# Performance work log

Hardware: AMD Instinct MI355X
Metric: run time of the kernel (lower is better)

The kernel has to match this reference:

```python
import jax, jax.numpy as jnp
import numpy as np

NUM_NODES = 50000
NUM_EDGES = 600000
IN_DIM = 128
OUT_DIM = 128


def setup_inputs() -> dict:
    key = jax.random.key(0)
    k1, k2, k3, k4, k5 = jax.random.split(key, 5)
    x = jax.random.normal(k1, (NUM_NODES, IN_DIM), dtype=jnp.float32)
    edge_index = jax.random.randint(k2, (2, NUM_EDGES), 0, NUM_NODES, dtype=jnp.int64)
    edge_weight = jax.random.uniform(k3, (NUM_EDGES,), dtype=jnp.float32)
    W = jax.random.normal(k4, (OUT_DIM, IN_DIM), dtype=jnp.float32) * (1.0 / np.sqrt(IN_DIM))
    b = jax.random.normal(k5, (OUT_DIM,), dtype=jnp.float32) * 0.01
    return {"x": x, "edge_index": edge_index, "edge_weight": edge_weight, "W": W, "b": b}


def reference(x, edge_index, edge_weight, W, b):
    num_nodes = x.shape[0]
    # add self loops
    loop = jnp.arange(num_nodes, dtype=edge_index.dtype)
    src = jnp.concatenate([edge_index[0], loop])           # [E + N]
    tgt = jnp.concatenate([edge_index[1], loop])           # [E + N]
    w = jnp.concatenate([edge_weight, jnp.ones((num_nodes,), dtype=edge_weight.dtype)])
    # degree via scatter-add over src, then symmetric normalization
    deg = jax.ops.segment_sum(w, src, num_segments=num_nodes)  # [N]
    dinv = 1.0 / jnp.sqrt(deg)
    w_norm = w * dinv[src] * dinv[tgt]                      # [E + N]
    # gather-scale-scatter aggregation
    msg = x[src] * w_norm[:, None]                          # [E + N, D]
    agg = jax.ops.segment_sum(msg, tgt, num_segments=num_nodes)  # [N, D]
    # dense linear (torch Linear convention)
    return agg @ W.T + b
```

## Files before the change

kernel.cpp:

```cpp
#include <hip/hip_runtime.h>

#define D 128
#define GROWS 32
#define HCHUNKS 64
#define RNG_H 8064
#define RNG_S 16128


__device__ __forceinline__ unsigned bf16rne(float f) {
  unsigned u = __float_as_uint(f);
  return (u + 0x7FFFu + ((u >> 16) & 1u)) >> 16;
}

__device__ __forceinline__ float4 bf16x4(uint2 u) {
  float4 r;
  r.x = __uint_as_float(u.x << 16);
  r.y = __uint_as_float(u.x & 0xFFFF0000u);
  r.z = __uint_as_float(u.y << 16);
  r.w = __uint_as_float(u.y & 0xFFFF0000u);
  return r;
}

__global__ __launch_bounds__(256) void k_setup(const float* __restrict__ W,
                                               const int* __restrict__ ei,
                                               float* __restrict__ Wt,
                                               int* __restrict__ flag) {
  int i = blockIdx.x * 256 + threadIdx.x;
  if (i < D * D) {
    int c = i >> 7, k = i & 127;
    Wt[k * D + c] = W[i];
  }
  if (i == 0) {
    flag[0] = (ei[1] == 0 && ei[3] == 0 && ei[5] == 0 && ei[7] == 0) ? 1 : 0;
  }
}

__global__ __launch_bounds__(256) void k_gemm(const float* __restrict__ x,
                                              const float* __restrict__ Wt,
                                              uint2* __restrict__ yb,
                                              int N) {
  __shared__ float Xs[GROWS * D];
  const int tid = threadIdx.x;
  const int row0 = blockIdx.x * GROWS;

  for (int f = tid; f < GROWS * D / 4; f += 256) {
    int r = row0 + ((f * 4) >> 7);
    float4 v = make_float4(0.f, 0.f, 0.f, 0.f);
    if (r < N)
      v = reinterpret_cast<const float4*>(x)[(size_t)row0 * (D / 4) + f];
    reinterpret_cast<float4*>(Xs)[f] = v;
  }
  __syncthreads();

  const int c0 = (tid & 31) * 4;
  const int r0 = (tid >> 5) * 4;
  float acc[4][4];
#pragma unroll
  for (int i = 0; i < 4; ++i)
#pragma unroll
    for (int j = 0; j < 4; ++j) acc[i][j] = 0.f;

#pragma unroll 4
  for (int k = 0; k < D; ++k) {
    float4 wv = reinterpret_cast<const float4*>(Wt)[(k * D + c0) >> 2];
    float xr[4];
#pragma unroll
    for (int i = 0; i < 4; ++i) xr[i] = Xs[(r0 + i) * D + k];
#pragma unroll
    for (int i = 0; i < 4; ++i) {
      acc[i][0] += xr[i] * wv.x;
      acc[i][1] += xr[i] * wv.y;
      acc[i][2] += xr[i] * wv.z;
      acc[i][3] += xr[i] * wv.w;
    }
  }
#pragma unroll
  for (int i = 0; i < 4; ++i) {
    int row = row0 + r0 + i;
    if (row < N) {
      uint2 u;
      u.x = bf16rne(acc[i][0]) | (bf16rne(acc[i][1]) << 16);
      u.y = bf16rne(acc[i][2]) | (bf16rne(acc[i][3]) << 16);
      yb[(size_t)row * 32 + (tid & 31)] = u;
    }
  }
}

__global__ __launch_bounds__(256) void k_hist(const int* __restrict__ ei,
                                              const float* __restrict__ ew,
                                              float* __restrict__ pdeg,
                                              int* __restrict__ pcnt,
                                              const int* __restrict__ flag,
                                              int E) {
  __shared__ float hd[RNG_H];
  __shared__ int hc[RNG_H];
  const int tid = threadIdx.x;
  const int chunk = blockIdx.x, r = blockIdx.y;
  const int lo = r * RNG_H;
  for (int i = tid; i < RNG_H; i += 256) { hd[i] = 0.f; hc[i] = 0; }
  __syncthreads();

  const int epc = (E + HCHUNKS - 1) / HCHUNKS;
  const int e0 = chunk * epc;
  const int e1 = min(e0 + epc, E);
  const bool f64 = flag[0] != 0;
  const int2* ei2 = reinterpret_cast<const int2*>(ei);
  for (int e = e0 + tid; e < e1; e += 256) {
    int s = f64 ? ei2[e].x : ei[e];
    int t = f64 ? ei2[E + e].x : ei[E + e];
    int ds = s - lo;
    if ((unsigned)ds < (unsigned)RNG_H) atomicAdd(&hd[ds], ew[e]);
    int dt = t - lo;
    if ((unsigned)dt < (unsigned)RNG_H) atomicAdd(&hc[dt], 1);
  }
  __syncthreads();
  size_t base = ((size_t)r * HCHUNKS + chunk) * RNG_H;
  for (int i = tid; i < RNG_H; i += 256) {
    pdeg[base + i] = hd[i];
    pcnt[base + i] = hc[i];
  }
}

__device__ __forceinline__ int wave_incl_scan(int v, int lane) {
#pragma unroll
  for (int o = 1; o < 64; o <<= 1) {
    int t = __shfl_up(v, o);
    if (lane >= o) v += t;
  }
  return v;
}

__global__ __launch_bounds__(256) void k_scan1(const float* __restrict__ pdeg,
                                               const int* __restrict__ pcnt,
                                               float* __restrict__ dinv,
                                               int* __restrict__ rowptr,
                                               int* __restrict__ blocksum,
                                               int N) {
  __shared__ int wtot[4];
  int tid = threadIdx.x;
  int i = blockIdx.x * 256 + tid;
  int v = 0;
  if (i < N) {
    int r = i / RNG_H, off = i - r * RNG_H;
    size_t base = (size_t)r * HCHUNKS * RNG_H + off;
    float s = 0.f;
    int c = 0;
#pragma unroll 8
    for (int k = 0; k < HCHUNKS; ++k) {
      s += pdeg[base + (size_t)k * RNG_H];
      c += pcnt[base + (size_t)k * RNG_H];
    }
    dinv[i] = rsqrtf(s + 1.0f);
    v = c;
  }
  int lane = tid & 63, wv = tid >> 6;
  int inc = wave_incl_scan(v, lane);
  if (lane == 63) wtot[wv] = inc;
  __syncthreads();
  if (tid == 0) {
    int r = 0;
#pragma unroll
    for (int k = 0; k < 4; ++k) { int t = wtot[k]; wtot[k] = r; r += t; }
  }
  __syncthreads();
  int exc = wtot[wv] + inc - v;
  if (i < N) rowptr[i] = exc;
  if (tid == 255) blocksum[blockIdx.x] = wtot[3] + inc;
}

__global__ __launch_bounds__(64) void k_scan2(int* __restrict__ blocksum,
                                              int* __restrict__ blockoff,
                                              int nb) {
  int lane = threadIdx.x;
  int carry = 0;
  for (int base = 0; base < nb; base += 64) {
    int idx = base + lane;
    int v = (idx < nb) ? blocksum[idx] : 0;
    int inc = wave_incl_scan(v, lane);
    if (idx < nb) blockoff[idx] = carry + inc - v;
    carry += __shfl(inc, 63);
  }
}

__global__ __launch_bounds__(256) void k_scan3base(int* __restrict__ rowptr,
                                                   const int* __restrict__ blockoff,
                                                   const int* __restrict__ pcnt,
                                                   int* __restrict__ cbase,
                                                   int N, int E) {
  int i = blockIdx.x * 256 + threadIdx.x;
  if (i >= N) {
    if (i == N) rowptr[N] = E;
    return;
  }
  int rp = rowptr[i] + blockoff[blockIdx.x];
  rowptr[i] = rp;
  if (i == 0) rowptr[N] = E;
  int r = i / RNG_H, off = i - r * RNG_H;
  size_t pb = (size_t)r * HCHUNKS * RNG_H + off;
  int run = rp;
#pragma unroll 8
  for (int c = 0; c < HCHUNKS; ++c) {
    cbase[(size_t)c * N + i] = run;
    run += pcnt[pb + (size_t)c * RNG_H];
  }
}

__global__ __launch_bounds__(256) void k_scatter(const int* __restrict__ ei,
                                                 const float* __restrict__ ew,
                                                 const float* __restrict__ dinv,
                                                 const int* __restrict__ cbase,
                                                 int2* __restrict__ edges,
                                                 const int* __restrict__ flag,
                                                 int N, int E) {
  __shared__ int hb[RNG_S];
  const int tid = threadIdx.x;
  const int chunk = blockIdx.x, r = blockIdx.y;
  const int lo = r * RNG_S;
  for (int j = tid; j < RNG_S; j += 256) {
    int v = lo + j;
    hb[j] = (v < N) ? cbase[(size_t)chunk * N + v] : 0;
  }
  __syncthreads();

  const int epc = (E + HCHUNKS - 1) / HCHUNKS;
  const int e0 = chunk * epc;
  const int e1 = min(e0 + epc, E);
  const bool f64 = flag[0] != 0;
  const int2* ei2 = reinterpret_cast<const int2*>(ei);
  for (int e = e0 + tid; e < e1; e += 256) {
    int t = f64 ? ei2[E + e].x : ei[E + e];
    int dt = t - lo;
    if ((unsigned)dt < (unsigned)RNG_S) {
      int s = f64 ? ei2[e].x : ei[e];
      int pos = atomicAdd(&hb[dt], 1);
      edges[pos] = make_int2(s, __float_as_int(ew[e] * dinv[s]));
    }
  }
}

__global__ __launch_bounds__(256) void k_gather(const int* __restrict__ rowptr,
                                                const int2* __restrict__ edges,
                                                const uint2* __restrict__ yb,
                                                const float* __restrict__ dinv,
                                                const float* __restrict__ b,
                                                float* __restrict__ out,
                                                int N) {
  const int tid = threadIdx.x;
  const int node = blockIdx.x * 4 + (tid >> 6);
  if (node >= N) return;
  const int lane = tid & 63, half = lane >> 5, l32 = lane & 31;

  const float dt = dinv[node];
  const float4 yself = bf16x4(yb[(size_t)node * 32 + l32]);
  const float4 bb = reinterpret_cast<const float4*>(b)[l32];

  float4 acc = make_float4(0.f, 0.f, 0.f, 0.f);
  const int end = rowptr[node + 1];
  int e = rowptr[node] + half;
  for (; e + 6 < end; e += 8) {
    int2 e0 = edges[e], e1 = edges[e + 2], e2 = edges[e + 4], e3 = edges[e + 6];
    float4 v0 = bf16x4(yb[(size_t)e0.x * 32 + l32]);
    float4 v1 = bf16x4(yb[(size_t)e1.x * 32 + l32]);
    float4 v2 = bf16x4(yb[(size_t)e2.x * 32 + l32]);
    float4 v3 = bf16x4(yb[(size_t)e3.x * 32 + l32]);
    float w0 = __int_as_float(e0.y), w1 = __int_as_float(e1.y);
    float w2 = __int_as_float(e2.y), w3 = __int_as_float(e3.y);
    acc.x += w0 * v0.x; acc.y += w0 * v0.y; acc.z += w0 * v0.z; acc.w += w0 * v0.w;
    acc.x += w1 * v1.x; acc.y += w1 * v1.y; acc.z += w1 * v1.z; acc.w += w1 * v1.w;
    acc.x += w2 * v2.x; acc.y += w2 * v2.y; acc.z += w2 * v2.z; acc.w += w2 * v2.w;
    acc.x += w3 * v3.x; acc.y += w3 * v3.y; acc.z += w3 * v3.z; acc.w += w3 * v3.w;
  }
  for (; e < end; e += 2) {
    int2 e0 = edges[e];
    float4 v0 = bf16x4(yb[(size_t)e0.x * 32 + l32]);
    float w0 = __int_as_float(e0.y);
    acc.x += w0 * v0.x; acc.y += w0 * v0.y; acc.z += w0 * v0.z; acc.w += w0 * v0.w;
  }
  acc.x += __shfl(acc.x, l32 + 32);
  acc.y += __shfl(acc.y, l32 + 32);
  acc.z += __shfl(acc.z, l32 + 32);
  acc.w += __shfl(acc.w, l32 + 32);
  if (half == 0) {
    float4 r;
    r.x = bb.x + dt * (acc.x + dt * yself.x);
    r.y = bb.y + dt * (acc.y + dt * yself.y);
    r.z = bb.z + dt * (acc.z + dt * yself.z);
    r.w = bb.w + dt * (acc.w + dt * yself.w);
    reinterpret_cast<float4*>(out)[(size_t)node * 32 + l32] = r;
  }
}

extern "C" void kernel_launch(void* const* d_in, const int* in_sizes, int n_in,
                              void* d_out, int out_size, void* d_ws, size_t ws_size,
                              hipStream_t stream) {
  const float* x = (const float*)d_in[0];
  const int* ei = (const int*)d_in[1];
  const float* ew = (const float*)d_in[2];
  const float* W = (const float*)d_in[3];
  const float* b = (const float*)d_in[4];
  float* out = (float*)d_out;

  const int N = in_sizes[0] / D;
  const int E = in_sizes[2];
  const int NB = (N + 255) / 256;
  const int nrH = (N + RNG_H - 1) / RNG_H;
  const int nrS = (N + RNG_S - 1) / RNG_S;

  char* ws = (char*)d_ws;
  size_t off = 0;
  auto alloc = [&](size_t bytes) {
    char* p = ws + off;
    off = (off + bytes + 255) & ~(size_t)255;
    return p;
  };
  float* Wt = (float*)alloc((size_t)D * D * 4);
  uint2* yb = (uint2*)alloc((size_t)N * D * 2);
  float* dinv = (float*)alloc((size_t)N * 4);
  float* pdeg = (float*)alloc((size_t)nrH * HCHUNKS * RNG_H * 4);
  int* pcnt = (int*)alloc((size_t)nrH * HCHUNKS * RNG_H * 4);
  int* cbase = (int*)alloc((size_t)HCHUNKS * N * 4);
  int* rowptr = (int*)alloc((size_t)(N + 1) * 4);
  int* blocksum = (int*)alloc((size_t)NB * 4);
  int* blockoff = (int*)alloc((size_t)NB * 4);
  int2* edges = (int2*)alloc((size_t)E * 8);
  int* flag = (int*)alloc(4);

  hipLaunchKernelGGL(k_setup, dim3((D * D + 255) / 256), dim3(256), 0, stream,
                     W, ei, Wt, flag);
  hipLaunchKernelGGL(k_gemm, dim3((N + GROWS - 1) / GROWS), dim3(256), 0,
                     stream, x, Wt, yb, N);
  hipLaunchKernelGGL(k_hist, dim3(HCHUNKS, nrH), dim3(256), 0, stream,
                     ei, ew, pdeg, pcnt, flag, E);
  hipLaunchKernelGGL(k_scan1, dim3(NB), dim3(256), 0, stream,
                     pdeg, pcnt, dinv, rowptr, blocksum, N);
  hipLaunchKernelGGL(k_scan2, dim3(1), dim3(64), 0, stream,
                     blocksum, blockoff, NB);
  hipLaunchKernelGGL(k_scan3base, dim3(NB), dim3(256), 0, stream,
                     rowptr, blockoff, pcnt, cbase, N, E);
  hipLaunchKernelGGL(k_scatter, dim3(HCHUNKS, nrS), dim3(256), 0, stream,
                     ei, ew, dinv, cbase, edges, flag, N, E);
  hipLaunchKernelGGL(k_gather, dim3((N + 3) / 4), dim3(256), 0, stream,
                     rowptr, edges, yb, dinv, b, out, N);
}
```

Baseline: 229.8 us.

## Double edge chunks, unify histogram/scatter node ranges, store partial counts as u16

Raises the number of edge chunks from 64 to 128 and gives the scatter kernel the same node range as the histogram kernel, so both launch more blocks. Per-chunk partial counts are now stored as 16-bit values, which halves the traffic for that buffer. The rowptr[N] write is moved to an extra scan block. In exchange, the per-chunk cbase and pdeg buffers double in size, scan1 and scan3base loop over twice as many chunks, and each scatter block re-reads its edge chunk for more node ranges.

```diff
diff --git a/kernel.cpp b/kernel.cpp
--- a/kernel.cpp
+++ b/kernel.cpp
@@ -2,9 +2,8 @@
 
 #define D 128
 #define GROWS 32
-#define HCHUNKS 64
-#define RNG_H 8064
-#define RNG_S 16128
+#define HCHUNKS 128
+#define RNG 8064
 
 
 __device__ __forceinline__ unsigned bf16rne(float f) {
@@ -89,15 +88,15 @@
 __global__ __launch_bounds__(256) void k_hist(const int* __restrict__ ei,
                                               const float* __restrict__ ew,
                                               float* __restrict__ pdeg,
-                                              int* __restrict__ pcnt,
+                                              unsigned short* __restrict__ pcnt,
                                               const int* __restrict__ flag,
                                               int E) {
-  __shared__ float hd[RNG_H];
-  __shared__ int hc[RNG_H];
+  __shared__ float hd[RNG];
+  __shared__ int hc[RNG];
   const int tid = threadIdx.x;
   const int chunk = blockIdx.x, r = blockIdx.y;
-  const int lo = r * RNG_H;
-  for (int i = tid; i < RNG_H; i += 256) { hd[i] = 0.f; hc[i] = 0; }
+  const int lo = r * RNG;
+  for (int i = tid; i < RNG; i += 256) { hd[i] = 0.f; hc[i] = 0; }
   __syncthreads();
 
   const int epc = (E + HCHUNKS - 1) / HCHUNKS;
@@ -109,15 +108,15 @@
     int s = f64 ? ei2[e].x : ei[e];
     int t = f64 ? ei2[E + e].x : ei[E + e];
     int ds = s - lo;
-    if ((unsigned)ds < (unsigned)RNG_H) atomicAdd(&hd[ds], ew[e]);
+    if ((unsigned)ds < (unsigned)RNG) atomicAdd(&hd[ds], ew[e]);
     int dt = t - lo;
-    if ((unsigned)dt < (unsigned)RNG_H) atomicAdd(&hc[dt], 1);
-  }
-  __syncthreads();
-  size_t base = ((size_t)r * HCHUNKS + chunk) * RNG_H;
-  for (int i = tid; i < RNG_H; i += 256) {
+    if ((unsigned)dt < (unsigned)RNG) atomicAdd(&hc[dt], 1);
+  }
+  __syncthreads();
+  size_t base = ((size_t)r * HCHUNKS + chunk) * RNG;
+  for (int i = tid; i < RNG; i += 256) {
     pdeg[base + i] = hd[i];
-    pcnt[base + i] = hc[i];
+    pcnt[base + i] = (unsigned short)hc[i];
   }
 }
 
@@ -131,7 +130,7 @@
 }
 
 __global__ __launch_bounds__(256) void k_scan1(const float* __restrict__ pdeg,
-                                               const int* __restrict__ pcnt,
+                                               const unsigned short* __restrict__ pcnt,
                                                float* __restrict__ dinv,
                                                int* __restrict__ rowptr,
                                                int* __restrict__ blocksum,
@@ -141,14 +140,14 @@
   int i = blockIdx.x * 256 + tid;
   int v = 0;
   if (i < N) {
-    int r = i / RNG_H, off = i - r * RNG_H;
-    size_t base = (size_t)r * HCHUNKS * RNG_H + off;
+    int r = i / RNG, off = i - r * RNG;
+    size_t base = (size_t)r * HCHUNKS * RNG + off;
     float s = 0.f;
     int c = 0;
 #pragma unroll 8
     for (int k = 0; k < HCHUNKS; ++k) {
-      s += pdeg[base + (size_t)k * RNG_H];
-      c += pcnt[base + (size_t)k * RNG_H];
+      s += pdeg[base + (size_t)k * RNG];
+      c += pcnt[base + (size_t)k * RNG];
     }
     dinv[i] = rsqrtf(s + 1.0f);
     v = c;
@@ -184,7 +183,7 @@
 
 __global__ __launch_bounds__(256) void k_scan3base(int* __restrict__ rowptr,
                                                    const int* __restrict__ blockoff,
-                                                   const int* __restrict__ pcnt,
+                                                   const unsigned short* __restrict__ pcnt,
                                                    int* __restrict__ cbase,
                                                    int N, int E) {
   int i = blockIdx.x * 256 + threadIdx.x;
@@ -194,14 +193,13 @@
   }
   int rp = rowptr[i] + blockoff[blockIdx.x];
   rowptr[i] = rp;
-  if (i == 0) rowptr[N] = E;
-  int r = i / RNG_H, off = i - r * RNG_H;
-  size_t pb = (size_t)r * HCHUNKS * RNG_H + off;
+  int r = i / RNG, off = i - r * RNG;
+  size_t pb = (size_t)r * HCHUNKS * RNG + off;
   int run = rp;
 #pragma unroll 8
   for (int c = 0; c < HCHUNKS; ++c) {
     cbase[(size_t)c * N + i] = run;
-    run += pcnt[pb + (size_t)c * RNG_H];
+    run += pcnt[pb + (size_t)c * RNG];
   }
 }
 
@@ -212,11 +210,11 @@
                                                  int2* __restrict__ edges,
                                                  const int* __restrict__ flag,
                                                  int N, int E) {
-  __shared__ int hb[RNG_S];
+  __shared__ int hb[RNG];
   const int tid = threadIdx.x;
   const int chunk = blockIdx.x, r = blockIdx.y;
-  const int lo = r * RNG_S;
-  for (int j = tid; j < RNG_S; j += 256) {
+  const int lo = r * RNG;
+  for (int j = tid; j < RNG; j += 256) {
     int v = lo + j;
     hb[j] = (v < N) ? cbase[(size_t)chunk * N + v] : 0;
   }
@@ -230,7 +228,7 @@
   for (int e = e0 + tid; e < e1; e += 256) {
     int t = f64 ? ei2[E + e].x : ei[E + e];
     int dt = t - lo;
-    if ((unsigned)dt < (unsigned)RNG_S) {
+    if ((unsigned)dt < (unsigned)RNG) {
       int s = f64 ? ei2[e].x : ei[e];
       int pos = atomicAdd(&hb[dt], 1);
       edges[pos] = make_int2(s, __float_as_int(ew[e] * dinv[s]));
@@ -303,8 +301,7 @@
   const int N = in_sizes[0] / D;
   const int E = in_sizes[2];
   const int NB = (N + 255) / 256;
-  const int nrH = (N + RNG_H - 1) / RNG_H;
-  const int nrS = (N + RNG_S - 1) / RNG_S;
+  const int nr = (N + RNG - 1) / RNG;
 
   char* ws = (char*)d_ws;
   size_t off = 0;
@@ -316,8 +313,9 @@
   float* Wt = (float*)alloc((size_t)D * D * 4);
   uint2* yb = (uint2*)alloc((size_t)N * D * 2);
   float* dinv = (float*)alloc((size_t)N * 4);
-  float* pdeg = (float*)alloc((size_t)nrH * HCHUNKS * RNG_H * 4);
-  int* pcnt = (int*)alloc((size_t)nrH * HCHUNKS * RNG_H * 4);
+  float* pdeg = (float*)alloc((size_t)nr * HCHUNKS * RNG * 4);
+  unsigned short* pcnt =
+      (unsigned short*)alloc((size_t)nr * HCHUNKS * RNG * 2);
   int* cbase = (int*)alloc((size_t)HCHUNKS * N * 4);
   int* rowptr = (int*)alloc((size_t)(N + 1) * 4);
   int* blocksum = (int*)alloc((size_t)NB * 4);
@@ -329,15 +327,15 @@
                      W, ei, Wt, flag);
   hipLaunchKernelGGL(k_gemm, dim3((N + GROWS - 1) / GROWS), dim3(256), 0,
                      stream, x, Wt, yb, N);
-  hipLaunchKernelGGL(k_hist, dim3(HCHUNKS, nrH), dim3(256), 0, stream,
+  hipLaunchKernelGGL(k_hist, dim3(HCHUNKS, nr), dim3(256), 0, stream,
                      ei, ew, pdeg, pcnt, flag, E);
   hipLaunchKernelGGL(k_scan1, dim3(NB), dim3(256), 0, stream,
                      pdeg, pcnt, dinv, rowptr, blocksum, N);
   hipLaunchKernelGGL(k_scan2, dim3(1), dim3(64), 0, stream,
                      blocksum, blockoff, NB);
-  hipLaunchKernelGGL(k_scan3base, dim3(NB), dim3(256), 0, stream,
+  hipLaunchKernelGGL(k_scan3base, dim3(NB + 1), dim3(256), 0, stream,
                      rowptr, blockoff, pcnt, cbase, N, E);
-  hipLaunchKernelGGL(k_scatter, dim3(HCHUNKS, nrS), dim3(256), 0, stream,
+  hipLaunchKernelGGL(k_scatter, dim3(HCHUNKS, nr), dim3(256), 0, stream,
                      ei, ew, dinv, cbase, edges, flag, N, E);
   hipLaunchKernelGGL(k_gather, dim3((N + 3) / 4), dim3(256), 0, stream,
                      rowptr, edges, yb, dinv, b, out, N);
```

Measured after the change: 223.0 us. -2.9%, faster.
